# Kernel optimization log

Measured on AMD Instinct MI355X. Metric: run time of the kernel, lower is better.

## Reference

```python
import jax, jax.numpy as jnp
import numpy as np

B, C, D = 8, 2048, 768
EPS = 1e-5


def setup_inputs() -> dict:
    key = jax.random.key(0)
    kx, kk, kq, kv = jax.random.split(key, 4)
    x = jax.random.normal(kx, (B, C, D), dtype=jnp.float32)
    # torch.nn.Linear(dim_in, dim_out, bias=False) -> weight [dim_out, dim_in]
    s = 1.0 / np.sqrt(D)
    Wk = jax.random.uniform(kk, (D, D), dtype=jnp.float32, minval=-s, maxval=s)
    Wq = jax.random.uniform(kq, (D, D), dtype=jnp.float32, minval=-s, maxval=s)
    Wv = jax.random.uniform(kv, (D, D), dtype=jnp.float32, minval=-s, maxval=s)
    return {"x": x, "Wk": Wk, "Wq": Wq, "Wv": Wv}


def reference(x, Wk, Wq, Wv):
    # LayerNorm over the last two dims [C, D] (fresh affine: gamma=1, beta=0)
    mean = jnp.mean(x, axis=(-2, -1), keepdims=True)
    var = jnp.mean(jnp.square(x - mean), axis=(-2, -1), keepdims=True)
    xn = (x - mean) * jax.lax.rsqrt(var + EPS)
    # Linear projections: y = x @ W.T
    keys = jnp.einsum('bcd,od->bco', xn, Wk)
    queries = jnp.einsum('bcd,od->bco', xn, Wq)
    values = jnp.einsum('bcd,od->bco', xn, Wv)
    # attention scores [B, C, C], softmax over keys axis (no 1/sqrt(d) in source)
    att = jax.nn.softmax(jnp.einsum('bid,bjd->bij', queries, keys), axis=-1)
    # out[b,i,d] = sum_j values[b,j,d] * att[b,i,j]
    return jnp.einsum('bjd,bij->bid', values, att)
```

## Files before the change

### kernel.cpp

```cpp
#include <hip/hip_runtime.h>
#include <stdint.h>

#define NB 8
#define NC 2048
#define ND 768
#define CD (NC * ND)
#define EPSV 1e-5f

typedef _Float16 f16;
typedef f16 f16x2 __attribute__((ext_vector_type(2)));
typedef f16 f16x8 __attribute__((ext_vector_type(8)));
typedef float f32x4 __attribute__((ext_vector_type(4)));
typedef unsigned short u16;
typedef unsigned int u32;
typedef u32 u32x2 __attribute__((ext_vector_type(2)));
typedef u32 u32x4 __attribute__((ext_vector_type(4)));

__device__ __forceinline__ u16 f2h(float f) {
  return __builtin_bit_cast(u16, (f16)f);
}
__device__ __forceinline__ u32 pack2(float a, float b) {
  f16x2 h = {(f16)a, (f16)b};
  return __builtin_bit_cast(u32, h);
}

__device__ __forceinline__ float wave_sum(float v) {
#pragma unroll
  for (int o = 32; o > 0; o >>= 1) v += __shfl_down(v, o);
  return v;
}
__device__ __forceinline__ float wave_max(float v) {
#pragma unroll
  for (int o = 32; o > 0; o >>= 1) v = fmaxf(v, __shfl_down(v, o));
  return v;
}

__global__ __launch_bounds__(256) void ln_stats(const float* __restrict__ x,
                                                float* __restrict__ stats) {
  const int b = blockIdx.y;
  const float4* xb = (const float4*)(x + (size_t)b * CD);
  const int base = blockIdx.x * 6144;
  float s1 = 0.f, s2 = 0.f;
  for (int i = threadIdx.x; i < 6144; i += 256) {
    float4 v = xb[base + i];
    s1 += (v.x + v.y) + (v.z + v.w);
    s2 += (v.x * v.x + v.y * v.y) + (v.z * v.z + v.w * v.w);
  }
  s1 = wave_sum(s1);
  s2 = wave_sum(s2);
  __shared__ float r1[4], r2[4];
  const int lane = threadIdx.x & 63, w = threadIdx.x >> 6;
  if (lane == 0) { r1[w] = s1; r2[w] = s2; }
  __syncthreads();
  if (threadIdx.x == 0) {
    atomicAdd(&stats[b * 2], (r1[0] + r1[1]) + (r1[2] + r1[3]));
    atomicAdd(&stats[b * 2 + 1], (r2[0] + r2[1]) + (r2[2] + r2[3]));
  }
}

__global__ __launch_bounds__(256) void ln_apply(const float* __restrict__ x,
                                                const float* __restrict__ stats,
                                                u16* __restrict__ xn) {
  const size_t i = ((size_t)blockIdx.x * 256 + threadIdx.x) * 8;
  const int b = (int)(i / CD);
  const float mean = stats[b * 2] * (1.f / CD);
  const float var = stats[b * 2 + 1] * (1.f / CD) - mean * mean;
  const float rstd = rsqrtf(var + EPSV);
  const float4 v0 = *(const float4*)(x + i);
  const float4 v1 = *(const float4*)(x + i + 4);
  u32x4 p;
  p.x = pack2((v0.x - mean) * rstd, (v0.y - mean) * rstd);
  p.y = pack2((v0.z - mean) * rstd, (v0.w - mean) * rstd);
  p.z = pack2((v1.x - mean) * rstd, (v1.y - mean) * rstd);
  p.w = pack2((v1.z - mean) * rstd, (v1.w - mean) * rstd);
  *(u32x4*)(xn + i) = p;
}

__global__ __launch_bounds__(256) void cast_w(const float* __restrict__ Wk,
                                              const float* __restrict__ Wq,
                                              const float* __restrict__ Wv,
                                              u16* __restrict__ Wb) {
  const size_t i = ((size_t)blockIdx.x * 256 + threadIdx.x) * 8;
  const size_t WSZ = (size_t)ND * ND;
  const float* src;
  size_t off;
  if (i < WSZ) { src = Wk; off = i; }
  else if (i < 2 * WSZ) { src = Wq; off = i - WSZ; }
  else { src = Wv; off = i - 2 * WSZ; }
  const float4 v0 = *(const float4*)(src + off);
  const float4 v1 = *(const float4*)(src + off + 4);
  u32x4 p;
  p.x = pack2(v0.x, v0.y);
  p.y = pack2(v0.z, v0.w);
  p.z = pack2(v1.x, v1.y);
  p.w = pack2(v1.z, v1.w);
  *(u32x4*)(Wb + i) = p;
}

__device__ __forceinline__ void stage_chunk(u16* dst, const u16* src, int ld, int tid) {
  const int rl = tid >> 2;
  const int sc = (tid & 3) ^ ((tid >> 3) & 3);
  const u16* gp = src + (size_t)rl * ld + sc * 8;
  __builtin_amdgcn_global_load_lds(
      (const __attribute__((address_space(1))) void*)gp,
      (__attribute__((address_space(3))) void*)(dst + tid * 8), 16, 0, 0);
}

__device__ __forceinline__ void mf16(f32x4 acc[8][4], int mb, const f16x8 a[4],
                                     const f16x8 b[4]) {
#pragma unroll
  for (int m = 0; m < 4; ++m)
#pragma unroll
    for (int n = 0; n < 4; ++n)
      acc[mb + m][n] =
          __builtin_amdgcn_mfma_f32_16x16x32_f16(a[m], b[n], acc[mb + m][n], 0, 0, 0);
}

__device__ __forceinline__ void gemm256(const u16* __restrict__ A, int lda,
                                        const u16* __restrict__ B, int ldb, int nk,
                                        u16 (*lds)[2][4][4096], int tid,
                                        f32x4 acc[8][4]) {
  const int lane = tid & 63;
  const int wc = (tid >> 6) & 3;
  const int wr = (tid >> 8) & 1;
  const int fr = lane & 15;
  const int SL = (lane >> 4) ^ ((lane >> 1) & 3);
  int aoff[4], boff[4];
#pragma unroll
  for (int m = 0; m < 4; ++m) aoff[m] = (wr * 64 + m * 16 + fr) * 32 + SL * 8;
#pragma unroll
  for (int n = 0; n < 4; ++n) boff[n] = (wc * 32 + (n & 1) * 16 + fr) * 32 + SL * 8;

#define STG_A(BUF, T, KK)                                                  \
  do {                                                                     \
    const u16* s_ = A + (size_t)(T) * 64 + (KK) * 32;                      \
    stage_chunk(&lds[BUF][0][(KK) * 2 + 0][0], s_, lda, tid);              \
    stage_chunk(&lds[BUF][0][(KK) * 2 + 1][0], s_ + (size_t)128 * lda, lda, tid); \
  } while (0)
#define STG_B(BUF, T, KK)                                                  \
  do {                                                                     \
    const u16* s_ = B + (size_t)(T) * 64 + (KK) * 32;                      \
    stage_chunk(&lds[BUF][1][(KK) * 2 + 0][0], s_, ldb, tid);              \
    stage_chunk(&lds[BUF][1][(KK) * 2 + 1][0], s_ + (size_t)128 * ldb, ldb, tid); \
  } while (0)

  STG_A(0, 0, 0); STG_B(0, 0, 0); STG_A(0, 0, 1); STG_B(0, 0, 1);

  for (int t = 0; t < nk; ++t) {
    const int cur = t & 1, nb = cur ^ 1;
    const bool pre = (t + 1 < nk);
    f16x8 a[4], b0[4], b1[4];
    asm volatile("s_waitcnt vmcnt(4)" ::: "memory");
    __builtin_amdgcn_s_barrier();
    __builtin_amdgcn_sched_barrier(0);
    if (pre) STG_A(nb, t + 1, 0);
#pragma unroll
    for (int m = 0; m < 4; ++m) a[m] = *(const f16x8*)&lds[cur][0][0][aoff[m]];
    b0[0] = *(const f16x8*)&lds[cur][1][0][boff[0]];
    b0[1] = *(const f16x8*)&lds[cur][1][0][boff[1]];
    b0[2] = *(const f16x8*)&lds[cur][1][1][boff[2]];
    b0[3] = *(const f16x8*)&lds[cur][1][1][boff[3]];
    __builtin_amdgcn_s_setprio(1);
    mf16(acc, 0, a, b0);
    __builtin_amdgcn_s_setprio(0);
    if (pre) STG_B(nb, t + 1, 0);
#pragma unroll
    for (int m = 0; m < 4; ++m) a[m] = *(const f16x8*)&lds[cur][0][1][aoff[m]];
    __builtin_amdgcn_s_setprio(1);
    mf16(acc, 4, a, b0);
    __builtin_amdgcn_s_setprio(0);
    if (pre) { asm volatile("s_waitcnt vmcnt(4)" ::: "memory"); }
    else     { asm volatile("s_waitcnt vmcnt(0)" ::: "memory"); }
    __builtin_amdgcn_s_barrier();
    __builtin_amdgcn_sched_barrier(0);
    if (pre) STG_A(nb, t + 1, 1);
#pragma unroll
    for (int m = 0; m < 4; ++m) a[m] = *(const f16x8*)&lds[cur][0][3][aoff[m]];
    b1[0] = *(const f16x8*)&lds[cur][1][2][boff[0]];
    b1[1] = *(const f16x8*)&lds[cur][1][2][boff[1]];
    b1[2] = *(const f16x8*)&lds[cur][1][3][boff[2]];
    b1[3] = *(const f16x8*)&lds[cur][1][3][boff[3]];
    __builtin_amdgcn_s_setprio(1);
    mf16(acc, 4, a, b1);
    __builtin_amdgcn_s_setprio(0);
    if (pre) STG_B(nb, t + 1, 1);
#pragma unroll
    for (int m = 0; m < 4; ++m) a[m] = *(const f16x8*)&lds[cur][0][2][aoff[m]];
    __builtin_amdgcn_s_setprio(1);
    mf16(acc, 0, a, b1);
    __builtin_amdgcn_s_setprio(0);
  }
#undef STG_A
#undef STG_B
}

__global__ __launch_bounds__(512, 1) void gemm_proj(const u16* __restrict__ xn,
                                                    const u16* __restrict__ Wb,
                                                    u16* __restrict__ Kb,
                                                    u16* __restrict__ Qb,
                                                    u16* __restrict__ Vt) {
  __shared__ u16 lds[2][2][4][4096];
  const int tid = threadIdx.x;
  const int brow = blockIdx.x * 256;
  const int bcol = blockIdx.y * 256;
  const int z = blockIdx.z;
  f32x4 acc[8][4] = {};
  gemm256(xn + (size_t)brow * ND, ND, Wb + (size_t)z * ND * ND + (size_t)bcol * ND, ND,
          ND / 64, lds, tid, acc);
  const int lane = tid & 63, wc = (tid >> 6) & 3, wr = (tid >> 8) & 1;
  if (z < 2) {
    u16* O = (z == 0) ? Kb : Qb;
#pragma unroll
    for (int mm = 0; mm < 8; ++mm) {
      const int r = brow + (mm >> 2) * 128 + wr * 64 + (mm & 3) * 16 + ((lane >> 4) << 2);
#pragma unroll
      for (int nn = 0; nn < 4; ++nn) {
        const int c = bcol + (nn >> 1) * 128 + wc * 32 + (nn & 1) * 16 + (lane & 15);
#pragma unroll
        for (int q = 0; q < 4; ++q) O[(size_t)(r + q) * ND + c] = f2h(acc[mm][nn][q]);
      }
    }
  } else {
#pragma unroll
    for (int mm = 0; mm < 8; ++mm) {
      const int r = brow + (mm >> 2) * 128 + wr * 64 + (mm & 3) * 16 + ((lane >> 4) << 2);
      const int bb = r >> 11;
      const int cc = r & 2047;
#pragma unroll
      for (int nn = 0; nn < 4; ++nn) {
        const int c = bcol + (nn >> 1) * 128 + wc * 32 + (nn & 1) * 16 + (lane & 15);
        u32x2 p;
        p.x = pack2(acc[mm][nn][0], acc[mm][nn][1]);
        p.y = pack2(acc[mm][nn][2], acc[mm][nn][3]);
        *(u32x2*)(Vt + ((size_t)bb * ND + c) * NC + cc) = p;
      }
    }
  }
}

__global__ __launch_bounds__(512, 1) void gemm_qk(const u16* __restrict__ Qb,
                                                  const u16* __restrict__ Kb,
                                                  float* __restrict__ S) {
  __shared__ u16 lds[2][2][4][4096];
  const int tid = threadIdx.x;
  const int bz = blockIdx.z;
  f32x4 acc[8][4] = {};
  gemm256(Qb + ((size_t)bz * NC + blockIdx.x * 256) * ND, ND,
          Kb + ((size_t)bz * NC + blockIdx.y * 256) * ND, ND, ND / 64, lds, tid, acc);
  float* Sb = S + (size_t)bz * NC * NC;
  const int lane = tid & 63, wc = (tid >> 6) & 3, wr = (tid >> 8) & 1;
#pragma unroll
  for (int mm = 0; mm < 8; ++mm) {
    const int r = blockIdx.x * 256 + (mm >> 2) * 128 + wr * 64 + (mm & 3) * 16 + ((lane >> 4) << 2);
#pragma unroll
    for (int nn = 0; nn < 4; ++nn) {
      const int c = blockIdx.y * 256 + (nn >> 1) * 128 + wc * 32 + (nn & 1) * 16 + (lane & 15);
#pragma unroll
      for (int q = 0; q < 4; ++q) Sb[(size_t)(r + q) * NC + c] = acc[mm][nn][q];
    }
  }
}

__global__ __launch_bounds__(256) void softmax_rows(float* __restrict__ S) {
  float* Sr = S + (size_t)blockIdx.x * NC;
  const int t = threadIdx.x;
  const float4* Sv = (const float4*)Sr;
  const float4 v0 = Sv[2 * t];
  const float4 v1 = Sv[2 * t + 1];
  float mv = fmaxf(fmaxf(fmaxf(v0.x, v0.y), fmaxf(v0.z, v0.w)),
                   fmaxf(fmaxf(v1.x, v1.y), fmaxf(v1.z, v1.w)));
  mv = wave_max(mv);
  __shared__ float rm[4], rs[4];
  const int lane = t & 63, w = t >> 6;
  if (lane == 0) rm[w] = mv;
  __syncthreads();
  const float bm = fmaxf(fmaxf(rm[0], rm[1]), fmaxf(rm[2], rm[3]));
  const float e0 = __expf(v0.x - bm), e1 = __expf(v0.y - bm);
  const float e2 = __expf(v0.z - bm), e3 = __expf(v0.w - bm);
  const float e4 = __expf(v1.x - bm), e5 = __expf(v1.y - bm);
  const float e6 = __expf(v1.z - bm), e7 = __expf(v1.w - bm);
  float s = ((e0 + e1) + (e2 + e3)) + ((e4 + e5) + (e6 + e7));
  s = wave_sum(s);
  if (lane == 0) rs[w] = s;
  __syncthreads();
  const float inv = 1.f / ((rs[0] + rs[1]) + (rs[2] + rs[3]));
  u32x4 p;
  p.x = pack2(e0 * inv, e1 * inv);
  p.y = pack2(e2 * inv, e3 * inv);
  p.z = pack2(e4 * inv, e5 * inv);
  p.w = pack2(e6 * inv, e7 * inv);
  u16* ar = (u16*)Sr;
  *(u32x4*)(ar + t * 8) = p;
}

__global__ __launch_bounds__(512, 1) void gemm_av(const u16* __restrict__ att,
                                                  const u16* __restrict__ Vt,
                                                  float* __restrict__ out) {
  __shared__ u16 lds[2][2][4][4096];
  const int tid = threadIdx.x;
  const int bz = blockIdx.z;
  f32x4 acc[8][4] = {};
  gemm256(att + ((size_t)bz * NC + blockIdx.x * 256) * (NC * 2), NC * 2,
          Vt + ((size_t)bz * ND + blockIdx.y * 256) * NC, NC, NC / 64, lds, tid, acc);
  float* Ob = out + (size_t)bz * NC * ND;
  const int lane = tid & 63, wc = (tid >> 6) & 3, wr = (tid >> 8) & 1;
#pragma unroll
  for (int mm = 0; mm < 8; ++mm) {
    const int r = blockIdx.x * 256 + (mm >> 2) * 128 + wr * 64 + (mm & 3) * 16 + ((lane >> 4) << 2);
#pragma unroll
    for (int nn = 0; nn < 4; ++nn) {
      const int c = blockIdx.y * 256 + (nn >> 1) * 128 + wc * 32 + (nn & 1) * 16 + (lane & 15);
#pragma unroll
      for (int q = 0; q < 4; ++q) Ob[(size_t)(r + q) * ND + c] = acc[mm][nn][q];
    }
  }
}

extern "C" void kernel_launch(void* const* d_in, const int* in_sizes, int n_in,
                              void* d_out, int out_size, void* d_ws, size_t ws_size,
                              hipStream_t stream) {
  (void)in_sizes; (void)n_in; (void)out_size; (void)ws_size;
  const float* x = (const float*)d_in[0];
  const float* Wk = (const float*)d_in[1];
  const float* Wq = (const float*)d_in[2];
  const float* Wv = (const float*)d_in[3];
  char* ws = (char*)d_ws;
  float* stats = (float*)ws;
  u16* xn = (u16*)(ws + 256);
  u16* Wb = (u16*)(ws + 25166080);
  u16* Qb = (u16*)(ws + 28705024);
  u16* Kb = (u16*)(ws + 53870848);
  u16* Vt = (u16*)(ws + 79036672);
  float* S = (float*)(ws + 104202496);
  float* out = (float*)d_out;

  hipMemsetAsync(stats, 0, 64, stream);
  ln_stats<<<dim3(64, 8), 256, 0, stream>>>(x, stats);
  ln_apply<<<6144, 256, 0, stream>>>(x, stats, xn);
  cast_w<<<864, 256, 0, stream>>>(Wk, Wq, Wv, Wb);
  gemm_proj<<<dim3(64, 3, 3), 512, 0, stream>>>(xn, Wb, Kb, Qb, Vt);
  gemm_qk<<<dim3(8, 8, 8), 512, 0, stream>>>(Qb, Kb, S);
  softmax_rows<<<16384, 256, 0, stream>>>(S);
  gemm_av<<<dim3(8, 3, 8), 512, 0, stream>>>((const u16*)S, Vt, out);
}
```

Measured before the change: 367.9 us.

## Swap GEMM operands for vectorized transposed epilogues and store scores in fp16

The projection, QK and AV GEMMs swap their A and B operands so each lane's four accumulator values are contiguous in the output, which lets the epilogues issue packed 8-byte or 16-byte stores instead of scalar strided ones. The QK score matrix is written as fp16 instead of fp32, halving score-matrix traffic, and the softmax reads fp16 in place. The GEMM main loop is also reordered to issue both A and B prefetches together and load both A halves before back-to-back MFMA groups. In exchange, raw logits are rounded to fp16 before the softmax, which costs precision and can overflow for large scores.

```diff
diff --git a/kernel.cpp b/kernel.cpp
--- a/kernel.cpp
+++ b/kernel.cpp
@@ -131,16 +131,16 @@
 #pragma unroll
   for (int n = 0; n < 4; ++n) boff[n] = (wc * 32 + (n & 1) * 16 + fr) * 32 + SL * 8;
 
-#define STG_A(BUF, T, KK)                                                  \
-  do {                                                                     \
-    const u16* s_ = A + (size_t)(T) * 64 + (KK) * 32;                      \
-    stage_chunk(&lds[BUF][0][(KK) * 2 + 0][0], s_, lda, tid);              \
+#define STG_A(BUF, T, KK)                                                         \
+  do {                                                                            \
+    const u16* s_ = A + (size_t)(T) * 64 + (KK) * 32;                             \
+    stage_chunk(&lds[BUF][0][(KK) * 2 + 0][0], s_, lda, tid);                     \
     stage_chunk(&lds[BUF][0][(KK) * 2 + 1][0], s_ + (size_t)128 * lda, lda, tid); \
   } while (0)
-#define STG_B(BUF, T, KK)                                                  \
-  do {                                                                     \
-    const u16* s_ = B + (size_t)(T) * 64 + (KK) * 32;                      \
-    stage_chunk(&lds[BUF][1][(KK) * 2 + 0][0], s_, ldb, tid);              \
+#define STG_B(BUF, T, KK)                                                         \
+  do {                                                                            \
+    const u16* s_ = B + (size_t)(T) * 64 + (KK) * 32;                             \
+    stage_chunk(&lds[BUF][1][(KK) * 2 + 0][0], s_, ldb, tid);                     \
     stage_chunk(&lds[BUF][1][(KK) * 2 + 1][0], s_ + (size_t)128 * ldb, ldb, tid); \
   } while (0)
 
@@ -149,45 +149,39 @@
   for (int t = 0; t < nk; ++t) {
     const int cur = t & 1, nb = cur ^ 1;
     const bool pre = (t + 1 < nk);
-    f16x8 a[4], b0[4], b1[4];
+    f16x8 a0[4], a1[4], b[4];
     asm volatile("s_waitcnt vmcnt(4)" ::: "memory");
     __builtin_amdgcn_s_barrier();
     __builtin_amdgcn_sched_barrier(0);
-    if (pre) STG_A(nb, t + 1, 0);
-#pragma unroll
-    for (int m = 0; m < 4; ++m) a[m] = *(const f16x8*)&lds[cur][0][0][aoff[m]];
-    b0[0] = *(const f16x8*)&lds[cur][1][0][boff[0]];
-    b0[1] = *(const f16x8*)&lds[cur][1][0][boff[1]];
-    b0[2] = *(const f16x8*)&lds[cur][1][1][boff[2]];
-    b0[3] = *(const f16x8*)&lds[cur][1][1][boff[3]];
+    if (pre) { STG_A(nb, t + 1, 0); STG_B(nb, t + 1, 0); }
+#pragma unroll
+    for (int m = 0; m < 4; ++m) a0[m] = *(const f16x8*)&lds[cur][0][0][aoff[m]];
+#pragma unroll
+    for (int m = 0; m < 4; ++m) a1[m] = *(const f16x8*)&lds[cur][0][1][aoff[m]];
+    b[0] = *(const f16x8*)&lds[cur][1][0][boff[0]];
+    b[1] = *(const f16x8*)&lds[cur][1][0][boff[1]];
+    b[2] = *(const f16x8*)&lds[cur][1][1][boff[2]];
+    b[3] = *(const f16x8*)&lds[cur][1][1][boff[3]];
     __builtin_amdgcn_s_setprio(1);
-    mf16(acc, 0, a, b0);
-    __builtin_amdgcn_s_setprio(0);
-    if (pre) STG_B(nb, t + 1, 0);
-#pragma unroll
-    for (int m = 0; m < 4; ++m) a[m] = *(const f16x8*)&lds[cur][0][1][aoff[m]];
-    __builtin_amdgcn_s_setprio(1);
-    mf16(acc, 4, a, b0);
+    mf16(acc, 0, a0, b);
+    mf16(acc, 4, a1, b);
     __builtin_amdgcn_s_setprio(0);
     if (pre) { asm volatile("s_waitcnt vmcnt(4)" ::: "memory"); }
     else     { asm volatile("s_waitcnt vmcnt(0)" ::: "memory"); }
     __builtin_amdgcn_s_barrier();
     __builtin_amdgcn_sched_barrier(0);
-    if (pre) STG_A(nb, t + 1, 1);
-#pragma unroll
-    for (int m = 0; m < 4; ++m) a[m] = *(const f16x8*)&lds[cur][0][3][aoff[m]];
-    b1[0] = *(const f16x8*)&lds[cur][1][2][boff[0]];
-    b1[1] = *(const f16x8*)&lds[cur][1][2][boff[1]];
-    b1[2] = *(const f16x8*)&lds[cur][1][3][boff[2]];
-    b1[3] = *(const f16x8*)&lds[cur][1][3][boff[3]];
+    if (pre) { STG_A(nb, t + 1, 1); STG_B(nb, t + 1, 1); }
+#pragma unroll
+    for (int m = 0; m < 4; ++m) a0[m] = *(const f16x8*)&lds[cur][0][2][aoff[m]];
+#pragma unroll
+    for (int m = 0; m < 4; ++m) a1[m] = *(const f16x8*)&lds[cur][0][3][aoff[m]];
+    b[0] = *(const f16x8*)&lds[cur][1][2][boff[0]];
+    b[1] = *(const f16x8*)&lds[cur][1][2][boff[1]];
+    b[2] = *(const f16x8*)&lds[cur][1][3][boff[2]];
+    b[3] = *(const f16x8*)&lds[cur][1][3][boff[3]];
     __builtin_amdgcn_s_setprio(1);
-    mf16(acc, 4, a, b1);
-    __builtin_amdgcn_s_setprio(0);
-    if (pre) STG_B(nb, t + 1, 1);
-#pragma unroll
-    for (int m = 0; m < 4; ++m) a[m] = *(const f16x8*)&lds[cur][0][2][aoff[m]];
-    __builtin_amdgcn_s_setprio(1);
-    mf16(acc, 0, a, b1);
+    mf16(acc, 0, a0, b);
+    mf16(acc, 4, a1, b);
     __builtin_amdgcn_s_setprio(0);
   }
 #undef STG_A
@@ -201,38 +195,42 @@
                                                     u16* __restrict__ Vt) {
   __shared__ u16 lds[2][2][4][4096];
   const int tid = threadIdx.x;
-  const int brow = blockIdx.x * 256;
-  const int bcol = blockIdx.y * 256;
+  const int xblk = blockIdx.x * 256;
+  const int wblk = blockIdx.y * 256;
   const int z = blockIdx.z;
   f32x4 acc[8][4] = {};
-  gemm256(xn + (size_t)brow * ND, ND, Wb + (size_t)z * ND * ND + (size_t)bcol * ND, ND,
-          ND / 64, lds, tid, acc);
   const int lane = tid & 63, wc = (tid >> 6) & 3, wr = (tid >> 8) & 1;
   if (z < 2) {
+    gemm256(Wb + (size_t)z * ND * ND + (size_t)wblk * ND, ND, xn + (size_t)xblk * ND, ND,
+            ND / 64, lds, tid, acc);
     u16* O = (z == 0) ? Kb : Qb;
 #pragma unroll
     for (int mm = 0; mm < 8; ++mm) {
-      const int r = brow + (mm >> 2) * 128 + wr * 64 + (mm & 3) * 16 + ((lane >> 4) << 2);
+      const int d = wblk + (mm >> 2) * 128 + wr * 64 + (mm & 3) * 16 + ((lane >> 4) << 2);
 #pragma unroll
       for (int nn = 0; nn < 4; ++nn) {
-        const int c = bcol + (nn >> 1) * 128 + wc * 32 + (nn & 1) * 16 + (lane & 15);
-#pragma unroll
-        for (int q = 0; q < 4; ++q) O[(size_t)(r + q) * ND + c] = f2h(acc[mm][nn][q]);
+        const int c = xblk + (nn >> 1) * 128 + wc * 32 + (nn & 1) * 16 + (lane & 15);
+        u32x2 p;
+        p.x = pack2(acc[mm][nn][0], acc[mm][nn][1]);
+        p.y = pack2(acc[mm][nn][2], acc[mm][nn][3]);
+        *(u32x2*)(O + (size_t)c * ND + d) = p;
       }
     }
   } else {
+    gemm256(xn + (size_t)xblk * ND, ND, Wb + (size_t)2 * ND * ND + (size_t)wblk * ND, ND,
+            ND / 64, lds, tid, acc);
 #pragma unroll
     for (int mm = 0; mm < 8; ++mm) {
-      const int r = brow + (mm >> 2) * 128 + wr * 64 + (mm & 3) * 16 + ((lane >> 4) << 2);
+      const int r = xblk + (mm >> 2) * 128 + wr * 64 + (mm & 3) * 16 + ((lane >> 4) << 2);
       const int bb = r >> 11;
       const int cc = r & 2047;
 #pragma unroll
       for (int nn = 0; nn < 4; ++nn) {
-        const int c = bcol + (nn >> 1) * 128 + wc * 32 + (nn & 1) * 16 + (lane & 15);
+        const int d = wblk + (nn >> 1) * 128 + wc * 32 + (nn & 1) * 16 + (lane & 15);
         u32x2 p;
         p.x = pack2(acc[mm][nn][0], acc[mm][nn][1]);
         p.y = pack2(acc[mm][nn][2], acc[mm][nn][3]);
-        *(u32x2*)(Vt + ((size_t)bb * ND + c) * NC + cc) = p;
+        *(u32x2*)(Vt + ((size_t)bb * ND + d) * NC + cc) = p;
       }
     }
   }
@@ -240,57 +238,59 @@
 
 __global__ __launch_bounds__(512, 1) void gemm_qk(const u16* __restrict__ Qb,
                                                   const u16* __restrict__ Kb,
-                                                  float* __restrict__ S) {
+                                                  u16* __restrict__ S) {
   __shared__ u16 lds[2][2][4][4096];
   const int tid = threadIdx.x;
   const int bz = blockIdx.z;
+  const int iblk = blockIdx.x * 256, jblk = blockIdx.y * 256;
   f32x4 acc[8][4] = {};
-  gemm256(Qb + ((size_t)bz * NC + blockIdx.x * 256) * ND, ND,
-          Kb + ((size_t)bz * NC + blockIdx.y * 256) * ND, ND, ND / 64, lds, tid, acc);
-  float* Sb = S + (size_t)bz * NC * NC;
+  gemm256(Kb + ((size_t)bz * NC + jblk) * ND, ND, Qb + ((size_t)bz * NC + iblk) * ND, ND,
+          ND / 64, lds, tid, acc);
+  u16* Sb = S + (size_t)bz * NC * NC;
   const int lane = tid & 63, wc = (tid >> 6) & 3, wr = (tid >> 8) & 1;
 #pragma unroll
   for (int mm = 0; mm < 8; ++mm) {
-    const int r = blockIdx.x * 256 + (mm >> 2) * 128 + wr * 64 + (mm & 3) * 16 + ((lane >> 4) << 2);
+    const int j = jblk + (mm >> 2) * 128 + wr * 64 + (mm & 3) * 16 + ((lane >> 4) << 2);
 #pragma unroll
     for (int nn = 0; nn < 4; ++nn) {
-      const int c = blockIdx.y * 256 + (nn >> 1) * 128 + wc * 32 + (nn & 1) * 16 + (lane & 15);
-#pragma unroll
-      for (int q = 0; q < 4; ++q) Sb[(size_t)(r + q) * NC + c] = acc[mm][nn][q];
+      const int i = iblk + (nn >> 1) * 128 + wc * 32 + (nn & 1) * 16 + (lane & 15);
+      u32x2 p;
+      p.x = pack2(acc[mm][nn][0], acc[mm][nn][1]);
+      p.y = pack2(acc[mm][nn][2], acc[mm][nn][3]);
+      *(u32x2*)(Sb + (size_t)i * NC + j) = p;
     }
   }
 }
 
-__global__ __launch_bounds__(256) void softmax_rows(float* __restrict__ S) {
-  float* Sr = S + (size_t)blockIdx.x * NC;
+__global__ __launch_bounds__(256) void softmax_rows(u16* __restrict__ S) {
+  u16* Sr = S + (size_t)blockIdx.x * NC;
   const int t = threadIdx.x;
-  const float4* Sv = (const float4*)Sr;
-  const float4 v0 = Sv[2 * t];
-  const float4 v1 = Sv[2 * t + 1];
-  float mv = fmaxf(fmaxf(fmaxf(v0.x, v0.y), fmaxf(v0.z, v0.w)),
-                   fmaxf(fmaxf(v1.x, v1.y), fmaxf(v1.z, v1.w)));
+  const f16x8 v = *(const f16x8*)(Sr + t * 8);
+  float f[8];
+#pragma unroll
+  for (int j = 0; j < 8; ++j) f[j] = (float)v[j];
+  float mv = fmaxf(fmaxf(fmaxf(f[0], f[1]), fmaxf(f[2], f[3])),
+                   fmaxf(fmaxf(f[4], f[5]), fmaxf(f[6], f[7])));
   mv = wave_max(mv);
   __shared__ float rm[4], rs[4];
   const int lane = t & 63, w = t >> 6;
   if (lane == 0) rm[w] = mv;
   __syncthreads();
   const float bm = fmaxf(fmaxf(rm[0], rm[1]), fmaxf(rm[2], rm[3]));
-  const float e0 = __expf(v0.x - bm), e1 = __expf(v0.y - bm);
-  const float e2 = __expf(v0.z - bm), e3 = __expf(v0.w - bm);
-  const float e4 = __expf(v1.x - bm), e5 = __expf(v1.y - bm);
-  const float e6 = __expf(v1.z - bm), e7 = __expf(v1.w - bm);
-  float s = ((e0 + e1) + (e2 + e3)) + ((e4 + e5) + (e6 + e7));
+  float e[8];
+  float s = 0.f;
+#pragma unroll
+  for (int j = 0; j < 8; ++j) { e[j] = __expf(f[j] - bm); s += e[j]; }
   s = wave_sum(s);
   if (lane == 0) rs[w] = s;
   __syncthreads();
   const float inv = 1.f / ((rs[0] + rs[1]) + (rs[2] + rs[3]));
   u32x4 p;
-  p.x = pack2(e0 * inv, e1 * inv);
-  p.y = pack2(e2 * inv, e3 * inv);
-  p.z = pack2(e4 * inv, e5 * inv);
-  p.w = pack2(e6 * inv, e7 * inv);
-  u16* ar = (u16*)Sr;
-  *(u32x4*)(ar + t * 8) = p;
+  p.x = pack2(e[0] * inv, e[1] * inv);
+  p.y = pack2(e[2] * inv, e[3] * inv);
+  p.z = pack2(e[4] * inv, e[5] * inv);
+  p.w = pack2(e[6] * inv, e[7] * inv);
+  *(u32x4*)(Sr + t * 8) = p;
 }
 
 __global__ __launch_bounds__(512, 1) void gemm_av(const u16* __restrict__ att,
@@ -299,19 +299,19 @@
   __shared__ u16 lds[2][2][4][4096];
   const int tid = threadIdx.x;
   const int bz = blockIdx.z;
+  const int iblk = blockIdx.x * 256, dblk = blockIdx.y * 256;
   f32x4 acc[8][4] = {};
-  gemm256(att + ((size_t)bz * NC + blockIdx.x * 256) * (NC * 2), NC * 2,
-          Vt + ((size_t)bz * ND + blockIdx.y * 256) * NC, NC, NC / 64, lds, tid, acc);
-  float* Ob = out + (size_t)bz * NC * ND;
+  gemm256(Vt + ((size_t)bz * ND + dblk) * NC, NC, att + ((size_t)bz * NC + iblk) * NC, NC,
+          NC / 64, lds, tid, acc);
+  float* Ob = out + (size_t)bz * CD;
   const int lane = tid & 63, wc = (tid >> 6) & 3, wr = (tid >> 8) & 1;
 #pragma unroll
   for (int mm = 0; mm < 8; ++mm) {
-    const int r = blockIdx.x * 256 + (mm >> 2) * 128 + wr * 64 + (mm & 3) * 16 + ((lane >> 4) << 2);
+    const int d = dblk + (mm >> 2) * 128 + wr * 64 + (mm & 3) * 16 + ((lane >> 4) << 2);
 #pragma unroll
     for (int nn = 0; nn < 4; ++nn) {
-      const int c = blockIdx.y * 256 + (nn >> 1) * 128 + wc * 32 + (nn & 1) * 16 + (lane & 15);
-#pragma unroll
-      for (int q = 0; q < 4; ++q) Ob[(size_t)(r + q) * ND + c] = acc[mm][nn][q];
+      const int i = iblk + (nn >> 1) * 128 + wc * 32 + (nn & 1) * 16 + (lane & 15);
+      *(f32x4*)(Ob + (size_t)i * ND + d) = acc[mm][nn];
     }
   }
 }
@@ -331,7 +331,7 @@
   u16* Qb = (u16*)(ws + 28705024);
   u16* Kb = (u16*)(ws + 53870848);
   u16* Vt = (u16*)(ws + 79036672);
-  float* S = (float*)(ws + 104202496);
+  u16* S = (u16*)(ws + 104202496);
   float* out = (float*)d_out;
 
   hipMemsetAsync(stats, 0, 64, stream);
@@ -341,5 +341,5 @@
   gemm_proj<<<dim3(64, 3, 3), 512, 0, stream>>>(xn, Wb, Kb, Qb, Vt);
   gemm_qk<<<dim3(8, 8, 8), 512, 0, stream>>>(Qb, Kb, S);
   softmax_rows<<<16384, 256, 0, stream>>>(S);
-  gemm_av<<<dim3(8, 3, 8), 512, 0, stream>>>((const u16*)S, Vt, out);
-}
+  gemm_av<<<dim3(8, 3, 8), 512, 0, stream>>>(S, Vt, out);
+}
```

Measured after the change: 356.6 us. 1.03x faster.
